# Optimization experiments

Measured on AMD Instinct MI355X. Metric: run time of the kernel, lower is better.

Reference implementation:

```python
import jax, jax.numpy as jnp
import numpy as np

B, Q, T, C = 2, 300, 25, 256
NH, NL, NP = 8, 4, 4
DFF = 1024
HD = C // NH
SHAPES = [(128, 128), (64, 64), (32, 32), (16, 16)]  # (H_l, W_l) per level
S = sum(h * w for h, w in SHAPES)
LQ = Q * T


def setup_inputs() -> dict:
    key = jax.random.key(0)
    ks = jax.random.split(key, 16)
    rn = lambda k, shape, s=0.02: jax.random.normal(k, shape, jnp.float32) * s
    starts = np.cumsum([0] + [h * w for h, w in SHAPES[:-1]])
    return {
        "tgt_text": jax.random.normal(ks[0], (B, Q, T, C), jnp.float32),
        "query_pos_text": jax.random.normal(ks[1], (B, Q, T, C), jnp.float32),
        "reference_points": jax.random.uniform(ks[2], (B, LQ, NL, 2), jnp.float32),
        "src": jax.random.normal(ks[3], (B, S, C), jnp.float32),
        "src_spatial_shapes": jnp.array(SHAPES, jnp.int32),
        "level_start_index": jnp.array(starts, jnp.int32),
        "in_proj_w": rn(ks[4], (3 * C, C)), "in_proj_b": jnp.zeros((3 * C,), jnp.float32),
        "out_proj_w": rn(ks[5], (C, C)), "out_proj_b": jnp.zeros((C,), jnp.float32),
        "ln1_g": jnp.ones((C,), jnp.float32), "ln1_b": jnp.zeros((C,), jnp.float32),
        "samp_off_w": rn(ks[6], (NH * NL * NP * 2, C)), "samp_off_b": rn(ks[7], (NH * NL * NP * 2,), 0.5),
        "aw_w": rn(ks[8], (NH * NL * NP, C)), "aw_b": jnp.zeros((NH * NL * NP,), jnp.float32),
        "vp_w": rn(ks[9], (C, C)), "vp_b": jnp.zeros((C,), jnp.float32),
        "op_w": rn(ks[10], (C, C)), "op_b": jnp.zeros((C,), jnp.float32),
        "ln2_g": jnp.ones((C,), jnp.float32), "ln2_b": jnp.zeros((C,), jnp.float32),
        "ffn1_w": rn(ks[11], (DFF, C)), "ffn1_b": jnp.zeros((DFF,), jnp.float32),
        "ffn2_w": rn(ks[12], (C, DFF)), "ffn2_b": jnp.zeros((C,), jnp.float32),
        "ln3_g": jnp.ones((C,), jnp.float32), "ln3_b": jnp.zeros((C,), jnp.float32),
    }


def _ln(x, g, b):
    m = jnp.mean(x, axis=-1, keepdims=True)
    v = jnp.var(x, axis=-1, keepdims=True)
    return (x - m) / jnp.sqrt(v + 1e-5) * g + b


def _self_attn(tgt, pos, in_proj_w, in_proj_b, out_proj_w, out_proj_b):
    # torch nn.MultiheadAttention math: q,k carry pos, v is raw tgt
    qk = (tgt + pos).reshape(B * Q, T, C)
    x = tgt.reshape(B * Q, T, C)
    Wq, Wk, Wv = jnp.split(in_proj_w, 3, axis=0)
    bq, bk, bv = jnp.split(in_proj_b, 3, axis=0)
    heads = lambda t: t.reshape(B * Q, T, NH, HD).transpose(0, 2, 1, 3)
    q = heads(qk @ Wq.T + bq)
    k = heads(qk @ Wk.T + bk)
    v = heads(x @ Wv.T + bv)
    attn = jax.nn.softmax(jnp.einsum("bhqd,bhkd->bhqk", q, k) / jnp.sqrt(jnp.float32(HD)), axis=-1)
    o = jnp.einsum("bhqk,bhkd->bhqd", attn, v).transpose(0, 2, 1, 3).reshape(B * Q, T, C)
    return (o @ out_proj_w.T + out_proj_b).reshape(B, Q, T, C)


def _ms_deform_attn(query, reference_points, src, shapes, samp_off_w, samp_off_b, aw_w, aw_b, vp_w, vp_b, op_w, op_b):
    # query: [B, LQ, C]; src: [B, S, C]
    value = (src @ vp_w.T + vp_b).reshape(B, S, NH, HD)
    off = (query @ samp_off_w.T + samp_off_b).reshape(B, LQ, NH, NL, NP, 2)
    aw = jax.nn.softmax((query @ aw_w.T + aw_b).reshape(B, LQ, NH, NL * NP), axis=-1)
    aw = aw.reshape(B, LQ, NH, NL, NP)
    # normalizer is (W_l, H_l)
    norm = jnp.array([[w, h] for (h, w) in shapes], jnp.float32)
    loc = reference_points[:, :, None, :, None, :] + off / norm[None, None, None, :, None, :]
    starts = np.cumsum([0] + [h * w for h, w in shapes])
    accum = jnp.zeros((B, NH, LQ, HD), jnp.float32)
    for l, (Hl, Wl) in enumerate(shapes):
        vl = value[:, starts[l]:starts[l] + Hl * Wl].transpose(0, 2, 1, 3)  # [B,NH,HW,HD]
        # grid_sample align_corners=False pixel coords
        xl = (loc[:, :, :, l, :, 0] * Wl - 0.5).transpose(0, 2, 1, 3).reshape(B, NH, LQ * NP)
        yl = (loc[:, :, :, l, :, 1] * Hl - 0.5).transpose(0, 2, 1, 3).reshape(B, NH, LQ * NP)
        x0 = jnp.floor(xl); y0 = jnp.floor(yl)
        wx1 = xl - x0; wy1 = yl - y0
        x0i = x0.astype(jnp.int32); y0i = y0.astype(jnp.int32)
        samp = jnp.zeros((B, NH, LQ * NP, HD), jnp.float32)
        for dx, dy, w in ((0, 0, (1 - wx1) * (1 - wy1)), (1, 0, wx1 * (1 - wy1)),
                          (0, 1, (1 - wx1) * wy1), (1, 1, wx1 * wy1)):
            xi = x0i + dx; yi = y0i + dy
            valid = (xi >= 0) & (xi < Wl) & (yi >= 0) & (yi < Hl)
            lin = jnp.clip(yi, 0, Hl - 1) * Wl + jnp.clip(xi, 0, Wl - 1)
            g = jnp.take_along_axis(vl, lin[..., None], axis=2)  # [B,NH,LQ*NP,HD]
            samp = samp + g * (w * valid)[..., None]
        samp = samp.reshape(B, NH, LQ, NP, HD)
        awl = aw[:, :, :, l, :].transpose(0, 2, 1, 3)  # [B,NH,LQ,NP]
        accum = accum + jnp.sum(samp * awl[..., None], axis=3)
    out = accum.transpose(0, 2, 1, 3).reshape(B, LQ, C)
    return out @ op_w.T + op_b


def reference(tgt_text, query_pos_text, reference_points, src, src_spatial_shapes, level_start_index,
              in_proj_w, in_proj_b, out_proj_w, out_proj_b, ln1_g, ln1_b,
              samp_off_w, samp_off_b, aw_w, aw_b, vp_w, vp_b, op_w, op_b, ln2_g, ln2_b,
              ffn1_w, ffn1_b, ffn2_w, ffn2_b, ln3_g, ln3_b):
    shapes = [tuple(int(v) for v in row) for row in np.asarray(src_spatial_shapes)]  # static
    # --- intra-text self-attention ---
    tgt2 = _self_attn(tgt_text, query_pos_text, in_proj_w, in_proj_b, out_proj_w, out_proj_b)
    tgt = _ln(tgt_text + tgt2, ln1_g, ln1_b)
    # --- multi-scale deformable cross-attention ---
    query = (tgt + query_pos_text).reshape(B, LQ, C)
    cross = _ms_deform_attn(query, reference_points, src, shapes,
                            samp_off_w, samp_off_b, aw_w, aw_b, vp_w, vp_b, op_w, op_b)
    tgt = _ln(tgt + cross.reshape(B, Q, T, C), ln2_g, ln2_b)
    # --- FFN ---
    ffn = jax.nn.relu(tgt @ ffn1_w.T + ffn1_b) @ ffn2_w.T + ffn2_b
    return _ln(tgt + ffn, ln3_g, ln3_b)
```

## Files before the change

### kernel.cpp

```cpp
#include <hip/hip_runtime.h>
#include <cstddef>

#define B_ 2
#define Q_ 300
#define T_ 25
#define C_ 256
#define NH_ 8
#define NL_ 4
#define NP_ 4
#define HD_ 32
#define DFF_ 1024
#define LQ_ (Q_ * T_)
#define NTOK_ (B_ * LQ_)
#define S_ 21760
#define BS_ (B_ * S_)

typedef __bf16 bf16x8 __attribute__((ext_vector_type(8)));
typedef float floatx4 __attribute__((ext_vector_type(4)));
typedef unsigned short ushort_t;

__device__ __forceinline__ unsigned pack_bf16(float x, float y) {
    unsigned ux = __float_as_uint(x) + 0x8000u;
    unsigned uy = __float_as_uint(y) + 0x8000u;
    return (ux >> 16) | (uy & 0xFFFF0000u);
}
__device__ __forceinline__ ushort_t f2bf_s(float x) {
    return (ushort_t)((__float_as_uint(x) + 0x8000u) >> 16);
}
__device__ __forceinline__ float bf2f(ushort_t u) {
    return __uint_as_float((unsigned)u << 16);
}

#define GBN 128
#define GBK 32
#define LDA_S 40

template<int AMODE, int OUT_BF16, int GBMT>
__global__ __launch_bounds__(256) void gemm_t(
    const void* __restrict__ Av, const float* __restrict__ A2,
    const float* __restrict__ W, const float* __restrict__ W2, int N1,
    const float* __restrict__ bias, const float* __restrict__ bias2,
    void* __restrict__ Cv, long long partStride,
    int M, int N, int K, int kChunk, int ldc, int relu)
{
    constexpr int LA = GBMT / 32;
    constexpr int WM = GBMT / 2;
    constexpr int NI = WM / 16;

    __shared__ unsigned short Asl[GBMT * LDA_S];
    __shared__ unsigned short Bsl[GBN * LDA_S];

    const int m0 = blockIdx.x * GBMT;
    const int n0 = blockIdx.y * GBN;
    const int z  = blockIdx.z;
    const int kbeg = z * kChunk;
    const int kend = min(K, kbeg + kChunk);

    const int t  = threadIdx.x;
    const int wid  = t >> 6;
    const int lane = t & 63;
    const int wm = (wid >> 1) * WM;
    const int wn = (wid & 1) * 64;
    const int fm = lane & 15;
    const int fq = (lane >> 4) * 8;

    floatx4 acc[NI][4];
    #pragma unroll
    for (int i = 0; i < NI; ++i)
        #pragma unroll
        for (int j = 0; j < 4; ++j)
            acc[i][j] = (floatx4){0.f, 0.f, 0.f, 0.f};

    float4 pa[LA];
    uint2  pab[LA];
    float4 pw[4];
    const float* Af = (const float*)Av;
    const ushort_t* Ab = (const ushort_t*)Av;

    auto load_tiles = [&](int k0) {
        #pragma unroll
        for (int i = 0; i < LA; ++i) {
            int idx = t + 256 * i;
            int row = idx >> 3;
            int c4  = (idx & 7) * 4;
            int gm = m0 + row;
            if constexpr (AMODE == 2) {
                uint2 v = {0u, 0u};
                if (gm < M) v = *(const uint2*)(Ab + (size_t)gm * K + k0 + c4);
                pab[i] = v;
            } else {
                float4 v = make_float4(0.f, 0.f, 0.f, 0.f);
                if (gm < M) {
                    v = *(const float4*)(Af + (size_t)gm * K + k0 + c4);
                    if constexpr (AMODE == 1) {
                        float4 v2 = *(const float4*)(A2 + (size_t)gm * K + k0 + c4);
                        v.x += v2.x; v.y += v2.y; v.z += v2.z; v.w += v2.w;
                    }
                }
                pa[i] = v;
            }
        }
        #pragma unroll
        for (int i = 0; i < 4; ++i) {
            int idx = t + 256 * i;
            int row = idx >> 3;
            int c4  = (idx & 7) * 4;
            int gn = n0 + row;
            const float* wr;
            if (W2 && gn >= N1) wr = W2 + (size_t)(gn - N1) * K;
            else                wr = W + (size_t)gn * K;
            pw[i] = *(const float4*)(wr + k0 + c4);
        }
    };

    load_tiles(kbeg);
    for (int k0 = kbeg; k0 < kend; k0 += GBK) {
        #pragma unroll
        for (int i = 0; i < LA; ++i) {
            int idx = t + 256 * i;
            int row = idx >> 3;
            int c4  = (idx & 7) * 4;
            if constexpr (AMODE == 2) {
                *(uint2*)&Asl[row * LDA_S + c4] = pab[i];
            } else {
                uint2 p;
                p.x = pack_bf16(pa[i].x, pa[i].y);
                p.y = pack_bf16(pa[i].z, pa[i].w);
                *(uint2*)&Asl[row * LDA_S + c4] = p;
            }
        }
        #pragma unroll
        for (int i = 0; i < 4; ++i) {
            int idx = t + 256 * i;
            int row = idx >> 3;
            int c4  = (idx & 7) * 4;
            uint2 q;
            q.x = pack_bf16(pw[i].x, pw[i].y);
            q.y = pack_bf16(pw[i].z, pw[i].w);
            *(uint2*)&Bsl[row * LDA_S + c4] = q;
        }
        __syncthreads();

        if (k0 + GBK < kend) load_tiles(k0 + GBK);

        bf16x8 af[NI], bfr[4];
        #pragma unroll
        for (int i = 0; i < NI; ++i)
            af[i] = *(const bf16x8*)&Asl[(wm + i * 16 + fm) * LDA_S + fq];
        #pragma unroll
        for (int j = 0; j < 4; ++j)
            bfr[j] = *(const bf16x8*)&Bsl[(wn + j * 16 + fm) * LDA_S + fq];

        #pragma unroll
        for (int i = 0; i < NI; ++i)
            #pragma unroll
            for (int j = 0; j < 4; ++j)
                acc[i][j] = __builtin_amdgcn_mfma_f32_16x16x32_bf16(af[i], bfr[j], acc[i][j], 0, 0, 0);
        __syncthreads();
    }

    float* Cf = (float*)Cv + (long long)z * partStride;
    ushort_t* Cb = (ushort_t*)Cv;
    const int cr = (lane >> 4) * 4;
    const int cc = lane & 15;
    #pragma unroll
    for (int j = 0; j < 4; ++j) {
        int gn = n0 + wn + j * 16 + cc;
        float bia = 0.f;
        if (z == 0) bia = (bias2 && gn >= N1) ? bias2[gn - N1] : bias[gn];
        #pragma unroll
        for (int i = 0; i < NI; ++i) {
            #pragma unroll
            for (int r = 0; r < 4; ++r) {
                int gm = m0 + wm + i * 16 + cr + r;
                if (gm < M) {
                    float v = acc[i][j][r] + bia;
                    if (relu) v = fmaxf(v, 0.f);
                    if constexpr (OUT_BF16) Cb[(size_t)gm * ldc + gn] = f2bf_s(v);
                    else                    Cf[(size_t)gm * ldc + gn] = v;
                }
            }
        }
    }
}

__global__ __launch_bounds__(64) void attn_kernel(
    const ushort_t* __restrict__ qkv,
    ushort_t* __restrict__ o)
{
    int sh = blockIdx.x;
    int s = sh >> 3, h = sh & 7;
    __shared__ float qs[T_][HD_], ks[T_][HD_], vs[T_][HD_];
    int t = threadIdx.x;

    for (int idx = t; idx < T_ * HD_; idx += 64) {
        int i = idx >> 5, d = idx & 31;
        size_t base = ((size_t)(s * T_ + i)) * 768 + h * HD_ + d;
        qs[i][d] = bf2f(qkv[base]);
        ks[i][d] = bf2f(qkv[base + 256]);
        vs[i][d] = bf2f(qkv[base + 512]);
    }
    __syncthreads();

    if (t < T_) {
        float sc[T_];
        float mx = -1e30f;
        #pragma unroll
        for (int j = 0; j < T_; ++j) {
            float dot = 0.f;
            #pragma unroll
            for (int d = 0; d < HD_; ++d) dot += qs[t][d] * ks[j][d];
            sc[j] = dot * 0.17677669529663687f;
            mx = fmaxf(mx, sc[j]);
        }
        float sum = 0.f;
        #pragma unroll
        for (int j = 0; j < T_; ++j) { sc[j] = __expf(sc[j] - mx); sum += sc[j]; }
        float inv = 1.f / sum;
        float out[HD_];
        #pragma unroll
        for (int d = 0; d < HD_; ++d) out[d] = 0.f;
        for (int j = 0; j < T_; ++j) {
            float p = sc[j] * inv;
            #pragma unroll
            for (int d = 0; d < HD_; ++d) out[d] += p * vs[j][d];
        }
        size_t ob = ((size_t)(s * T_ + t)) * C_ + h * HD_;
        #pragma unroll
        for (int d = 0; d < HD_; ++d) o[ob + d] = f2bf_s(out[d]);
    }
}

__global__ __launch_bounds__(256) void ln_kernel(
    const float* __restrict__ x, const float* __restrict__ r,
    int nparts, long long rstride,
    const float* __restrict__ g, const float* __restrict__ b,
    float* __restrict__ out, const float* __restrict__ pos,
    float* __restrict__ qout)
{
    int tok = blockIdx.x;
    int t = threadIdx.x;
    size_t base = (size_t)tok * C_;
    float v = x[base + t];
    for (int p = 0; p < nparts; ++p)
        v += r[(long long)base + t + (long long)p * rstride];

    float s = v, ss = v * v;
    #pragma unroll
    for (int off = 32; off; off >>= 1) {
        s += __shfl_down(s, off);
        ss += __shfl_down(ss, off);
    }
    __shared__ float ws[4], wss[4];
    __shared__ float mean_s, rstd_s;
    int wid = t >> 6, lane = t & 63;
    if (lane == 0) { ws[wid] = s; wss[wid] = ss; }
    __syncthreads();
    if (t == 0) {
        float S = 0.f, SS = 0.f;
        #pragma unroll
        for (int i = 0; i < 4; ++i) { S += ws[i]; SS += wss[i]; }
        float m = S / 256.f;
        float var = SS / 256.f - m * m;
        mean_s = m;
        rstd_s = rsqrtf(var + 1e-5f);
    }
    __syncthreads();
    float y = (v - mean_s) * rstd_s * g[t] + b[t];
    out[base + t] = y;
    if (qout) qout[base + t] = y + pos[base + t];
}

__global__ __launch_bounds__(256) void deform_kernel(
    const ushort_t* __restrict__ value,
    const float* __restrict__ d12,
    const float* __restrict__ refpts,
    ushort_t* __restrict__ out)
{
    const int lane = threadIdx.x & 63;
    const int wave = threadIdx.x >> 6;
    const int half = lane >> 5;
    const int tok = blockIdx.x * 8 + wave * 2 + half;
    const int h  = (lane >> 2) & 7;
    const int d8 = (lane & 3) * 8;
    const int b = tok / LQ_;

    const float* awp = d12 + (size_t)tok * 384 + 256 + h * 16;
    float logit[16];
    float mx = -1e30f;
    #pragma unroll
    for (int i = 0; i < 16; ++i) { logit[i] = awp[i]; mx = fmaxf(mx, logit[i]); }
    float sum = 0.f;
    #pragma unroll
    for (int i = 0; i < 16; ++i) { logit[i] = __expf(logit[i] - mx); sum += logit[i]; }
    float inv = 1.f / sum;

    const float* offp = d12 + (size_t)tok * 384 + h * 32;
    const float* refp = refpts + (size_t)tok * (NL_ * 2);

    const int HW[4]     = {128, 64, 32, 16};
    const int starts[4] = {0, 16384, 20480, 21504};

    float accv[8];
    #pragma unroll
    for (int i = 0; i < 8; ++i) accv[i] = 0.f;

    #pragma unroll
    for (int l = 0; l < 4; ++l) {
        const int Hl = HW[l], Wl = HW[l];
        float rx = refp[l * 2 + 0], ry = refp[l * 2 + 1];
        const ushort_t* vbase = value + ((size_t)b * S_ + starts[l]) * (NH_ * HD_) + h * HD_ + d8;
        #pragma unroll
        for (int p = 0; p < 4; ++p) {
            float ox = offp[(l * 4 + p) * 2 + 0];
            float oy = offp[(l * 4 + p) * 2 + 1];
            float xl = rx * (float)Wl + ox - 0.5f;
            float yl = ry * (float)Hl + oy - 0.5f;
            float x0f = floorf(xl), y0f = floorf(yl);
            int x0 = (int)x0f, y0 = (int)y0f;
            float wx1 = xl - x0f, wy1 = yl - y0f;
            float wx0 = 1.f - wx1, wy0 = 1.f - wy1;
            float aww = logit[l * 4 + p] * inv;

            #pragma unroll
            for (int c = 0; c < 4; ++c) {
                int dx = c & 1, dy = c >> 1;
                int xi = x0 + dx, yi = y0 + dy;
                float w = (dx ? wx1 : wx0) * (dy ? wy1 : wy0);
                bool valid = (xi >= 0) & (xi < Wl) & (yi >= 0) & (yi < Hl);
                int xc = min(max(xi, 0), Wl - 1);
                int yc = min(max(yi, 0), Hl - 1);
                float wc = (valid ? w : 0.f) * aww;
                uint4 raw = *(const uint4*)(vbase + ((size_t)(yc * Wl + xc)) * (NH_ * HD_));
                accv[0] += __uint_as_float((raw.x & 0xFFFFu) << 16) * wc;
                accv[1] += __uint_as_float(raw.x & 0xFFFF0000u) * wc;
                accv[2] += __uint_as_float((raw.y & 0xFFFFu) << 16) * wc;
                accv[3] += __uint_as_float(raw.y & 0xFFFF0000u) * wc;
                accv[4] += __uint_as_float((raw.z & 0xFFFFu) << 16) * wc;
                accv[5] += __uint_as_float(raw.z & 0xFFFF0000u) * wc;
                accv[6] += __uint_as_float((raw.w & 0xFFFFu) << 16) * wc;
                accv[7] += __uint_as_float(raw.w & 0xFFFF0000u) * wc;
            }
        }
    }
    uint4 po;
    po.x = pack_bf16(accv[0], accv[1]);
    po.y = pack_bf16(accv[2], accv[3]);
    po.z = pack_bf16(accv[4], accv[5]);
    po.w = pack_bf16(accv[6], accv[7]);
    *(uint4*)(out + (size_t)tok * C_ + h * HD_ + d8) = po;
}

extern "C" void kernel_launch(void* const* d_in, const int* in_sizes, int n_in,
                              void* d_out, int out_size, void* d_ws, size_t ws_size,
                              hipStream_t stream) {
    const float* tgt_text = (const float*)d_in[0];
    const float* pos      = (const float*)d_in[1];
    const float* refpts   = (const float*)d_in[2];
    const float* src      = (const float*)d_in[3];
    const float* in_proj_w  = (const float*)d_in[6];
    const float* in_proj_b  = (const float*)d_in[7];
    const float* out_proj_w = (const float*)d_in[8];
    const float* out_proj_b = (const float*)d_in[9];
    const float* ln1_g = (const float*)d_in[10];
    const float* ln1_b = (const float*)d_in[11];
    const float* samp_off_w = (const float*)d_in[12];
    const float* samp_off_b = (const float*)d_in[13];
    const float* aw_w = (const float*)d_in[14];
    const float* aw_b = (const float*)d_in[15];
    const float* vp_w = (const float*)d_in[16];
    const float* vp_b = (const float*)d_in[17];
    const float* op_w = (const float*)d_in[18];
    const float* op_b = (const float*)d_in[19];
    const float* ln2_g = (const float*)d_in[20];
    const float* ln2_b = (const float*)d_in[21];
    const float* ffn1_w = (const float*)d_in[22];
    const float* ffn1_b = (const float*)d_in[23];
    const float* ffn2_w = (const float*)d_in[24];
    const float* ffn2_b = (const float*)d_in[25];
    const float* ln3_g = (const float*)d_in[26];
    const float* ln3_b = (const float*)d_in[27];

    const long long NC = (long long)NTOK_ * C_;
    float* ws = (float*)d_ws;
    float* A    = ws;
    float* Bq   = ws + NC;
    float* Creg = ws + 2 * NC;
    float* D12  = Creg + (long long)NTOK_ * DFF_;
    float* E    = D12 + (long long)NTOK_ * 384;
    float* F    = E + NC;

    const int MB64  = (NTOK_ + 63) / 64;
    const int MB128 = (NTOK_ + 127) / 128;
    const int MBV64 = BS_ / 64;

    gemm_t<1, 1, 64><<<dim3(MB64, 4, 1), 256, 0, stream>>>(tgt_text, pos, in_proj_w, nullptr, 0,
        in_proj_b, nullptr, Creg, 0, NTOK_, 512, 256, 256, 768, 0);
    gemm_t<0, 1, 64><<<dim3(MB64, 2, 1), 256, 0, stream>>>(tgt_text, nullptr, in_proj_w + 512 * 256, nullptr, 0,
        in_proj_b + 512, nullptr, (void*)((ushort_t*)Creg + 512), 0, NTOK_, 256, 256, 256, 768, 0);
    attn_kernel<<<B_ * Q_ * NH_, 64, 0, stream>>>((const ushort_t*)Creg, (ushort_t*)E);
    gemm_t<2, 0, 64><<<dim3(MB64, 2, 1), 256, 0, stream>>>(E, nullptr, out_proj_w, nullptr, 0,
        out_proj_b, nullptr, F, 0, NTOK_, 256, 256, 256, 256, 0);
    ln_kernel<<<NTOK_, 256, 0, stream>>>(tgt_text, F, 1, 0,
                                         ln1_g, ln1_b, A, pos, Bq);
    gemm_t<0, 1, 64><<<dim3(MBV64, 2, 1), 256, 0, stream>>>(src, nullptr, vp_w, nullptr, 0,
        vp_b, nullptr, Creg, 0, BS_, 256, 256, 256, 256, 0);
    gemm_t<0, 0, 64><<<dim3(MB64, 3, 1), 256, 0, stream>>>(Bq, nullptr, samp_off_w, aw_w, 256,
        samp_off_b, aw_b, D12, 0, NTOK_, 384, 256, 256, 384, 0);
    deform_kernel<<<NTOK_ / 8, 256, 0, stream>>>((const ushort_t*)Creg, D12, refpts, (ushort_t*)E);
    gemm_t<2, 0, 64><<<dim3(MB64, 2, 1), 256, 0, stream>>>(E, nullptr, op_w, nullptr, 0,
        op_b, nullptr, F, 0, NTOK_, 256, 256, 256, 256, 0);
    ln_kernel<<<NTOK_, 256, 0, stream>>>(A, F, 1, 0,
                                         ln2_g, ln2_b, A, nullptr, nullptr);
    gemm_t<0, 1, 128><<<dim3(MB128, 8, 1), 256, 0, stream>>>(A, nullptr, ffn1_w, nullptr, 0,
        ffn1_b, nullptr, Creg, 0, NTOK_, DFF_, 256, 256, DFF_, 1);
    gemm_t<2, 0, 64><<<dim3(MB64, 2, 2), 256, 0, stream>>>(Creg, nullptr, ffn2_w, nullptr, 0,
        ffn2_b, nullptr, E, NC, NTOK_, 256, 1024, 512, 256, 0);
    ln_kernel<<<NTOK_, 256, 0, stream>>>(A, E, 2, NC,
                                         ln3_g, ln3_b, (float*)d_out, nullptr, nullptr);
}
```

Measured before the change: 454.4 us.

## Pre-convert weights to bf16, head-major value layout, wave-per-token layernorm

A new kernel converts all weight matrices to bf16 once per call, so the GEMMs load half the weight bytes and skip the per-tile packing. The value projection now writes its output head-major (batch, head, position, dim), so the deformable sampling gathers from a contiguous 32-wide slab per head. LayerNorm switches from one 256-thread block per token with shared-memory reductions to one wave per token using float4 loads and xor-shuffles. The cost is an extra launch and a workspace region for the bf16 weights.

```diff
diff --git a/kernel.cpp b/kernel.cpp
--- a/kernel.cpp
+++ b/kernel.cpp
@@ -31,15 +31,51 @@
     return __uint_as_float((unsigned)u << 16);
 }
 
+#define WOFF_IP   0
+#define WOFF_OUT  196608
+#define WOFF_VP   262144
+#define WOFF_SO   327680
+#define WOFF_AW   393216
+#define WOFF_OP   425984
+#define WOFF_F1   491520
+#define WOFF_F2   753664
+#define WTOTAL    1015808
+
+__global__ __launch_bounds__(256) void convw_kernel(
+    const float* __restrict__ ipw, const float* __restrict__ outw,
+    const float* __restrict__ vpw, const float* __restrict__ sampw,
+    const float* __restrict__ aww, const float* __restrict__ opw,
+    const float* __restrict__ f1w, const float* __restrict__ f2w,
+    ushort_t* __restrict__ dst)
+{
+    long long g = ((long long)blockIdx.x * 256 + threadIdx.x) * 8;
+    if (g >= WTOTAL) return;
+    const float* src; long long off;
+    if      (g < WOFF_OUT) { src = ipw;   off = WOFF_IP; }
+    else if (g < WOFF_VP)  { src = outw;  off = WOFF_OUT; }
+    else if (g < WOFF_SO)  { src = vpw;   off = WOFF_VP; }
+    else if (g < WOFF_AW)  { src = sampw; off = WOFF_SO; }
+    else if (g < WOFF_OP)  { src = aww;   off = WOFF_AW; }
+    else if (g < WOFF_F1)  { src = opw;   off = WOFF_OP; }
+    else if (g < WOFF_F2)  { src = f1w;   off = WOFF_F1; }
+    else                   { src = f2w;   off = WOFF_F2; }
+    const float4* s4 = (const float4*)(src + (g - off));
+    float4 a = s4[0], b = s4[1];
+    uint4 o;
+    o.x = pack_bf16(a.x, a.y); o.y = pack_bf16(a.z, a.w);
+    o.z = pack_bf16(b.x, b.y); o.w = pack_bf16(b.z, b.w);
+    *(uint4*)(dst + g) = o;
+}
+
 #define GBN 128
 #define GBK 32
 #define LDA_S 40
 
-template<int AMODE, int OUT_BF16, int GBMT>
-__global__ __launch_bounds__(256) void gemm_t(
+template<int AMODE, int OUTMODE, int GBMT>
+__global__ __launch_bounds__(256) void gemm_w(
     const void* __restrict__ Av, const float* __restrict__ A2,
-    const float* __restrict__ W, const float* __restrict__ W2, int N1,
-    const float* __restrict__ bias, const float* __restrict__ bias2,
+    const ushort_t* __restrict__ W,
+    const float* __restrict__ bias, const float* __restrict__ bias2, int N1,
     void* __restrict__ Cv, long long partStride,
     int M, int N, int K, int kChunk, int ldc, int relu)
 {
@@ -73,7 +109,7 @@
 
     float4 pa[LA];
     uint2  pab[LA];
-    float4 pw[4];
+    uint2  pwb[4];
     const float* Af = (const float*)Av;
     const ushort_t* Ab = (const ushort_t*)Av;
 
@@ -105,11 +141,7 @@
             int idx = t + 256 * i;
             int row = idx >> 3;
             int c4  = (idx & 7) * 4;
-            int gn = n0 + row;
-            const float* wr;
-            if (W2 && gn >= N1) wr = W2 + (size_t)(gn - N1) * K;
-            else                wr = W + (size_t)gn * K;
-            pw[i] = *(const float4*)(wr + k0 + c4);
+            pwb[i] = *(const uint2*)(W + (size_t)(n0 + row) * K + k0 + c4);
         }
     };
 
@@ -134,10 +166,7 @@
             int idx = t + 256 * i;
             int row = idx >> 3;
             int c4  = (idx & 7) * 4;
-            uint2 q;
-            q.x = pack_bf16(pw[i].x, pw[i].y);
-            q.y = pack_bf16(pw[i].z, pw[i].w);
-            *(uint2*)&Bsl[row * LDA_S + c4] = q;
+            *(uint2*)&Bsl[row * LDA_S + c4] = pwb[i];
         }
         __syncthreads();
 
@@ -176,8 +205,15 @@
                 if (gm < M) {
                     float v = acc[i][j][r] + bia;
                     if (relu) v = fmaxf(v, 0.f);
-                    if constexpr (OUT_BF16) Cb[(size_t)gm * ldc + gn] = f2bf_s(v);
-                    else                    Cf[(size_t)gm * ldc + gn] = v;
+                    if constexpr (OUTMODE == 2) {
+                        int bb = gm >= S_;
+                        int s  = gm - bb * S_;
+                        Cb[(((size_t)(bb * 8 + (gn >> 5))) * S_ + s) * 32 + (gn & 31)] = f2bf_s(v);
+                    } else if constexpr (OUTMODE == 1) {
+                        Cb[(size_t)gm * ldc + gn] = f2bf_s(v);
+                    } else {
+                        Cf[(size_t)gm * ldc + gn] = v;
+                    }
                 }
             }
         }
@@ -231,44 +267,48 @@
     }
 }
 
-__global__ __launch_bounds__(256) void ln_kernel(
+__global__ __launch_bounds__(256) void ln4_kernel(
     const float* __restrict__ x, const float* __restrict__ r,
     int nparts, long long rstride,
     const float* __restrict__ g, const float* __restrict__ b,
     float* __restrict__ out, const float* __restrict__ pos,
     float* __restrict__ qout)
 {
-    int tok = blockIdx.x;
-    int t = threadIdx.x;
-    size_t base = (size_t)tok * C_;
-    float v = x[base + t];
-    for (int p = 0; p < nparts; ++p)
-        v += r[(long long)base + t + (long long)p * rstride];
-
-    float s = v, ss = v * v;
-    #pragma unroll
-    for (int off = 32; off; off >>= 1) {
-        s += __shfl_down(s, off);
-        ss += __shfl_down(ss, off);
-    }
-    __shared__ float ws[4], wss[4];
-    __shared__ float mean_s, rstd_s;
-    int wid = t >> 6, lane = t & 63;
-    if (lane == 0) { ws[wid] = s; wss[wid] = ss; }
-    __syncthreads();
-    if (t == 0) {
-        float S = 0.f, SS = 0.f;
-        #pragma unroll
-        for (int i = 0; i < 4; ++i) { S += ws[i]; SS += wss[i]; }
-        float m = S / 256.f;
-        float var = SS / 256.f - m * m;
-        mean_s = m;
-        rstd_s = rsqrtf(var + 1e-5f);
-    }
-    __syncthreads();
-    float y = (v - mean_s) * rstd_s * g[t] + b[t];
-    out[base + t] = y;
-    if (qout) qout[base + t] = y + pos[base + t];
+    const int wave = threadIdx.x >> 6;
+    const int lane = threadIdx.x & 63;
+    const int tok = blockIdx.x * 4 + wave;
+    const size_t base = (size_t)tok * C_ + lane * 4;
+
+    float4 v = *(const float4*)(x + base);
+    for (int p = 0; p < nparts; ++p) {
+        float4 rv = *(const float4*)(r + base + (long long)p * rstride);
+        v.x += rv.x; v.y += rv.y; v.z += rv.z; v.w += rv.w;
+    }
+    float s  = v.x + v.y + v.z + v.w;
+    float ss = v.x * v.x + v.y * v.y + v.z * v.z + v.w * v.w;
+    #pragma unroll
+    for (int m = 32; m; m >>= 1) {
+        s  += __shfl_xor(s, m);
+        ss += __shfl_xor(ss, m);
+    }
+    float mean = s * (1.f / 256.f);
+    float var  = ss * (1.f / 256.f) - mean * mean;
+    float rstd = rsqrtf(var + 1e-5f);
+
+    float4 gv = *(const float4*)(g + lane * 4);
+    float4 bv = *(const float4*)(b + lane * 4);
+    float4 y;
+    y.x = (v.x - mean) * rstd * gv.x + bv.x;
+    y.y = (v.y - mean) * rstd * gv.y + bv.y;
+    y.z = (v.z - mean) * rstd * gv.z + bv.z;
+    y.w = (v.w - mean) * rstd * gv.w + bv.w;
+    *(float4*)(out + base) = y;
+    if (qout) {
+        float4 pv = *(const float4*)(pos + base);
+        float4 q;
+        q.x = y.x + pv.x; q.y = y.y + pv.y; q.z = y.z + pv.z; q.w = y.w + pv.w;
+        *(float4*)(qout + base) = q;
+    }
 }
 
 __global__ __launch_bounds__(256) void deform_kernel(
@@ -309,7 +349,7 @@
     for (int l = 0; l < 4; ++l) {
         const int Hl = HW[l], Wl = HW[l];
         float rx = refp[l * 2 + 0], ry = refp[l * 2 + 1];
-        const ushort_t* vbase = value + ((size_t)b * S_ + starts[l]) * (NH_ * HD_) + h * HD_ + d8;
+        const ushort_t* vbase = value + (((size_t)(b * 8 + h)) * S_ + starts[l]) * HD_ + d8;
         #pragma unroll
         for (int p = 0; p < 4; ++p) {
             float ox = offp[(l * 4 + p) * 2 + 0];
@@ -331,7 +371,7 @@
                 int xc = min(max(xi, 0), Wl - 1);
                 int yc = min(max(yi, 0), Hl - 1);
                 float wc = (valid ? w : 0.f) * aww;
-                uint4 raw = *(const uint4*)(vbase + ((size_t)(yc * Wl + xc)) * (NH_ * HD_));
+                uint4 raw = *(const uint4*)(vbase + (size_t)(yc * Wl + xc) * HD_);
                 accv[0] += __uint_as_float((raw.x & 0xFFFFu) << 16) * wc;
                 accv[1] += __uint_as_float(raw.x & 0xFFFF0000u) * wc;
                 accv[2] += __uint_as_float((raw.y & 0xFFFFu) << 16) * wc;
@@ -389,33 +429,39 @@
     float* D12  = Creg + (long long)NTOK_ * DFF_;
     float* E    = D12 + (long long)NTOK_ * 384;
     float* F    = E + NC;
+    ushort_t* wb = (ushort_t*)(F + NC);
+
+    ushort_t* qkv  = (ushort_t*)Creg;
+    ushort_t* valt = (ushort_t*)Creg + (size_t)NTOK_ * 768;
 
     const int MB64  = (NTOK_ + 63) / 64;
     const int MB128 = (NTOK_ + 127) / 128;
     const int MBV64 = BS_ / 64;
 
-    gemm_t<1, 1, 64><<<dim3(MB64, 4, 1), 256, 0, stream>>>(tgt_text, pos, in_proj_w, nullptr, 0,
-        in_proj_b, nullptr, Creg, 0, NTOK_, 512, 256, 256, 768, 0);
-    gemm_t<0, 1, 64><<<dim3(MB64, 2, 1), 256, 0, stream>>>(tgt_text, nullptr, in_proj_w + 512 * 256, nullptr, 0,
-        in_proj_b + 512, nullptr, (void*)((ushort_t*)Creg + 512), 0, NTOK_, 256, 256, 256, 768, 0);
-    attn_kernel<<<B_ * Q_ * NH_, 64, 0, stream>>>((const ushort_t*)Creg, (ushort_t*)E);
-    gemm_t<2, 0, 64><<<dim3(MB64, 2, 1), 256, 0, stream>>>(E, nullptr, out_proj_w, nullptr, 0,
-        out_proj_b, nullptr, F, 0, NTOK_, 256, 256, 256, 256, 0);
-    ln_kernel<<<NTOK_, 256, 0, stream>>>(tgt_text, F, 1, 0,
-                                         ln1_g, ln1_b, A, pos, Bq);
-    gemm_t<0, 1, 64><<<dim3(MBV64, 2, 1), 256, 0, stream>>>(src, nullptr, vp_w, nullptr, 0,
-        vp_b, nullptr, Creg, 0, BS_, 256, 256, 256, 256, 0);
-    gemm_t<0, 0, 64><<<dim3(MB64, 3, 1), 256, 0, stream>>>(Bq, nullptr, samp_off_w, aw_w, 256,
-        samp_off_b, aw_b, D12, 0, NTOK_, 384, 256, 256, 384, 0);
-    deform_kernel<<<NTOK_ / 8, 256, 0, stream>>>((const ushort_t*)Creg, D12, refpts, (ushort_t*)E);
-    gemm_t<2, 0, 64><<<dim3(MB64, 2, 1), 256, 0, stream>>>(E, nullptr, op_w, nullptr, 0,
-        op_b, nullptr, F, 0, NTOK_, 256, 256, 256, 256, 0);
-    ln_kernel<<<NTOK_, 256, 0, stream>>>(A, F, 1, 0,
-                                         ln2_g, ln2_b, A, nullptr, nullptr);
-    gemm_t<0, 1, 128><<<dim3(MB128, 8, 1), 256, 0, stream>>>(A, nullptr, ffn1_w, nullptr, 0,
-        ffn1_b, nullptr, Creg, 0, NTOK_, DFF_, 256, 256, DFF_, 1);
-    gemm_t<2, 0, 64><<<dim3(MB64, 2, 2), 256, 0, stream>>>(Creg, nullptr, ffn2_w, nullptr, 0,
-        ffn2_b, nullptr, E, NC, NTOK_, 256, 1024, 512, 256, 0);
-    ln_kernel<<<NTOK_, 256, 0, stream>>>(A, E, 2, NC,
-                                         ln3_g, ln3_b, (float*)d_out, nullptr, nullptr);
-}
+    convw_kernel<<<496, 256, 0, stream>>>(in_proj_w, out_proj_w, vp_w, samp_off_w,
+                                          aw_w, op_w, ffn1_w, ffn2_w, wb);
+    gemm_w<1, 1, 64><<<dim3(MB64, 4, 1), 256, 0, stream>>>(tgt_text, pos, wb + WOFF_IP,
+        in_proj_b, nullptr, 0, qkv, 0, NTOK_, 512, 256, 256, 768, 0);
+    gemm_w<0, 1, 64><<<dim3(MB64, 2, 1), 256, 0, stream>>>(tgt_text, nullptr, wb + WOFF_IP + 512 * 256,
+        in_proj_b + 512, nullptr, 0, qkv + 512, 0, NTOK_, 256, 256, 256, 768, 0);
+    gemm_w<0, 2, 64><<<dim3(MBV64, 2, 1), 256, 0, stream>>>(src, nullptr, wb + WOFF_VP,
+        vp_b, nullptr, 0, valt, 0, BS_, 256, 256, 256, 0, 0);
+    attn_kernel<<<B_ * Q_ * NH_, 64, 0, stream>>>(qkv, (ushort_t*)E);
+    gemm_w<2, 0, 64><<<dim3(MB64, 2, 1), 256, 0, stream>>>(E, nullptr, wb + WOFF_OUT,
+        out_proj_b, nullptr, 0, F, 0, NTOK_, 256, 256, 256, 256, 0);
+    ln4_kernel<<<NTOK_ / 4, 256, 0, stream>>>(tgt_text, F, 1, 0,
+                                              ln1_g, ln1_b, A, pos, Bq);
+    gemm_w<0, 0, 64><<<dim3(MB64, 3, 1), 256, 0, stream>>>(Bq, nullptr, wb + WOFF_SO,
+        samp_off_b, aw_b, 256, D12, 0, NTOK_, 384, 256, 256, 384, 0);
+    deform_kernel<<<NTOK_ / 8, 256, 0, stream>>>(valt, D12, refpts, (ushort_t*)E);
+    gemm_w<2, 0, 64><<<dim3(MB64, 2, 1), 256, 0, stream>>>(E, nullptr, wb + WOFF_OP,
+        op_b, nullptr, 0, F, 0, NTOK_, 256, 256, 256, 256, 0);
+    ln4_kernel<<<NTOK_ / 4, 256, 0, stream>>>(A, F, 1, 0,
+                                              ln2_g, ln2_b, A, nullptr, nullptr);
+    gemm_w<0, 1, 128><<<dim3(MB128, 8, 1), 256, 0, stream>>>(A, nullptr, wb + WOFF_F1,
+        ffn1_b, nullptr, 0, Creg, 0, NTOK_, DFF_, 256, 256, DFF_, 1);
+    gemm_w<2, 0, 64><<<dim3(MB64, 2, 2), 256, 0, stream>>>(Creg, nullptr, wb + WOFF_F2,
+        ffn2_b, nullptr, 0, E, NC, NTOK_, 256, 1024, 512, 256, 0);
+    ln4_kernel<<<NTOK_ / 4, 256, 0, stream>>>(A, E, 2, NC,
+                                              ln3_g, ln3_b, (float*)d_out, nullptr, nullptr);
+}
```

After: 421.9 us. 1.08x faster.
